# Kernel tuning notes

Hardware: AMD Instinct MI355X
Metric: run time of the kernel (lower is better)

Reference implementation:

```python
import jax, jax.numpy as jnp
import numpy as np

N = 30000   # clients (single instance, repeat=1)
F = 16      # num_node_features
EP = 30000  # solution-graph (tour) edges per parent
EF = 240000 # full graph k-NN edges (degree 8)
H = 8       # heads
D = 64      # hidden_dim
R = 64      # routes per parent (= max_to_move)
HD = H * D  # 512


def _gatv2(x, src, dst, ea, Wl, Wr, We, att, b, d_out):
    # PyG GATv2Conv: score = att . leaky_relu(Wl x_src + Wr x_dst + We e), softmax over dst
    n = x.shape[0]
    xl = (x @ Wl).reshape(n, H, d_out)
    xr = (x @ Wr).reshape(n, H, d_out)
    ee = (ea @ We).reshape(-1, H, d_out)
    s = jax.nn.leaky_relu(xl[src] + xr[dst] + ee, 0.2)          # [E,H,d]
    logits = jnp.einsum('ehd,hd->eh', s, att)                    # [E,H]
    m = jax.ops.segment_max(logits, dst, num_segments=n)
    ex = jnp.exp(logits - m[dst])
    den = jax.ops.segment_sum(ex, dst, num_segments=n)
    alpha = ex / (den[dst] + 1e-16)
    out = jax.ops.segment_sum(xl[src] * alpha[..., None], dst, num_segments=n)
    return out.reshape(n, H * d_out) + b


def _bn(x, g, b):
    # BatchNorm with track_running_stats=False -> batch statistics
    mu = jnp.mean(x, 0)
    v = jnp.var(x, 0)
    return (x - mu) * jax.lax.rsqrt(v + 1e-5) * g + b


def _routes(emb, rid):
    # sum client embeddings per route, then prefix sums over routes (moved vs kept sets)
    rs = jax.ops.segment_sum(emb, rid, num_segments=R)   # [R, 2HD]
    cs = jnp.cumsum(rs, 0)
    return cs, cs[-1] - cs


def setup_inputs() -> dict:
    key = jax.random.key(0)
    ks = iter(jax.random.split(key, 64))
    sc = 0.05
    rn = lambda shape: jax.random.normal(next(ks), shape, jnp.float32)
    d = {}
    d['x_p1'] = rn((N, F)); d['x_p2'] = rn((N, F)); d['x_full'] = rn((N, F))
    d['ea_p1'] = jax.random.uniform(next(ks), (EP, 1))
    d['ea_p2'] = jax.random.uniform(next(ks), (EP, 1))
    d['ea_full'] = jax.random.uniform(next(ks), (EF, 1))
    d['ei_p1'] = jax.random.randint(next(ks), (2, EP), 0, N)
    d['ei_p2'] = jax.random.randint(next(ks), (2, EP), 0, N)
    d['ei_full'] = jax.random.randint(next(ks), (2, EF), 0, N)
    d['route_p1'] = jax.random.randint(next(ks), (N,), 0, R)
    d['route_p2'] = jax.random.randint(next(ks), (N,), 0, R)
    # GAT params: (SolutionGraph, FullGraph, both)
    for tag, cin, dout in (('1', F, D), ('2', F, D), ('3', 2 * HD, 2 * D)):
        d['Wl' + tag] = rn((cin, H * dout)) * sc
        d['Wr' + tag] = rn((cin, H * dout)) * sc
        d['We' + tag] = rn((1, H * dout)) * sc
        d['att' + tag] = rn((H, dout)) * sc
        d['b' + tag] = jnp.zeros((H * dout,), jnp.float32)
    d['bng'] = jnp.ones((2 * HD,), jnp.float32); d['bnb'] = jnp.zeros((2 * HD,), jnp.float32)
    d['png'] = jnp.ones((8 * HD,), jnp.float32); d['pnb'] = jnp.zeros((8 * HD,), jnp.float32)
    dims = [8 * HD, 4 * HD, 2 * HD, HD, HD // 2, HD // 4, HD // 8, HD // 16, 1]
    for i in range(8):
        d['W%d' % (i + 1)] = rn((dims[i], dims[i + 1])) * sc
        d['c%d' % (i + 1)] = jnp.zeros((dims[i + 1],), jnp.float32)
    return d


def reference(x_p1, x_p2, x_full, ea_p1, ea_p2, ea_full, ei_p1, ei_p2, ei_full,
              route_p1, route_p2,
              Wl1, Wr1, We1, att1, b1, Wl2, Wr2, We2, att2, b2,
              Wl3, Wr3, We3, att3, b3, bng, bnb, png, pnb,
              W1, c1, W2, c2, W3, c3, W4, c4, W5, c5, W6, c6, W7, c7, W8, c8):
    p1 = _gatv2(x_p1, ei_p1[0], ei_p1[1], ea_p1, Wl1, Wr1, We1, att1, b1, D)
    p2 = _gatv2(x_p2, ei_p2[0], ei_p2[1], ea_p2, Wl1, Wr1, We1, att1, b1, D)
    fg = _gatv2(x_full, ei_full[0], ei_full[1], ea_full, Wl2, Wr2, We2, att2, b2, D)
    # single instance -> repeat=1: concat client embedding with full-graph embedding
    p1f = _bn(jnp.concatenate([p1, fg], 1), bng, bnb)
    p2f = _bn(jnp.concatenate([p2, fg], 1), bng, bnb)
    p1f = _gatv2(p1f, ei_p1[0], ei_p1[1], ea_p1, Wl3, Wr3, We3, att3, b3, 2 * D)
    p2f = _gatv2(p2f, ei_p2[0], ei_p2[1], ea_p2, Wl3, Wr3, We3, att3, b3, 2 * D)
    c1s, r1s = _routes(p1f, route_p1)
    c2s, r2s = _routes(p2f, route_p2)
    ptop = jnp.concatenate([c1s, r1s, c2s, r2s], 1)   # [R, 8*HD]
    h = _bn(ptop, png, pnb)
    lrelu = lambda z: jax.nn.leaky_relu(z, 0.01)
    h = lrelu(h @ W1 + c1)
    h = lrelu(h @ W2 + c2)
    h = lrelu(h @ W3 + c3)
    h = lrelu(h @ W4 + c4)
    h = lrelu(h @ W5 + c5)
    h = lrelu(h @ W6 + c6)
    h = lrelu(h @ W7 + c7)
    h = h @ W8 + c8
    probs = jax.nn.sigmoid(h).ravel()
    ptop_batch = jnp.zeros((R,), jnp.int32)
    return probs, ptop_batch
```

## Files before the change

### kernel.cpp

```cpp
#include <hip/hip_runtime.h>
#include <stdint.h>

typedef unsigned short u16;
typedef unsigned int   u32;
typedef __attribute__((ext_vector_type(8))) short bf16x8;
typedef __attribute__((ext_vector_type(4))) float f32x4;

#define NN    30000
#define NNP   30208
#define EFULL 240000
#define EPAR  30000

__device__ __forceinline__ float b2f(u16 u){ u32 x=((u32)u)<<16; float f; __builtin_memcpy(&f,&x,4); return f; }
__device__ __forceinline__ u16 f2b(float f){ u32 x; __builtin_memcpy(&x,&f,4); x += 0x7fffu + ((x>>16)&1u); return (u16)(x>>16); }

__device__ __forceinline__ void gload_lds16(const u16* g, u16* l){
  __builtin_amdgcn_global_load_lds((const __attribute__((address_space(1))) void*)g,
                                   (__attribute__((address_space(3))) void*)l, 16, 0, 0);
}

__global__ void k_fail(float* out){ int t=threadIdx.x; if(t<128) out[t]=2.0f; }

__global__ void k_counte3(const int* __restrict__ d0, const int* __restrict__ d1, const int* __restrict__ d2,
                          int* __restrict__ c0, int* __restrict__ c1, int* __restrict__ c2){
  int z = blockIdx.z;
  const int* d = z==0? d0 : z==1? d1 : d2;
  int* c = z==0? c0 : z==1? c1 : c2;
  int E = z==0? EFULL : EPAR;
  int e = blockIdx.x*256 + threadIdx.x;
  if (e < E) atomicAdd(&c[d[e]], 1);
}

__global__ void k_scan3(const int* __restrict__ c0, const int* __restrict__ c1, const int* __restrict__ c2,
                        int* __restrict__ r0, int* __restrict__ r1, int* __restrict__ r2,
                        int* __restrict__ w0, int* __restrict__ w1, int* __restrict__ w2){
  __shared__ int sums[1024];
  int z = blockIdx.x;
  const int* cnt = z==0? c0 : z==1? c1 : c2;
  int* rp = z==0? r0 : z==1? r1 : r2;
  int* wp = z==0? w0 : z==1? w1 : w2;
  int t = threadIdx.x;
  const int CH = (NN + 1023)/1024;
  int c00 = t*CH;
  int s = 0;
  for (int i=0;i<CH;i++){ int idx=c00+i; s += (idx<NN)? cnt[idx] : 0; }
  sums[t] = s; __syncthreads();
  for (int off=1; off<1024; off<<=1){
    int v = (t>=off)? sums[t-off] : 0;
    __syncthreads();
    sums[t] += v;
    __syncthreads();
  }
  int run = (t==0)? 0 : sums[t-1];
  for (int i=0;i<CH;i++){
    int idx=c00+i;
    if (idx<NN){ rp[idx]=run; wp[idx]=run; run += cnt[idx]; }
  }
  if (t==1023) rp[NN] = sums[1023];
}

__global__ void k_count64(const int* __restrict__ rt0, const int* __restrict__ rt1,
                          const int* __restrict__ d0, const int* __restrict__ d1,
                          int* __restrict__ c0, int* __restrict__ c1,
                          int* __restrict__ c2, int* __restrict__ c3){
  int z = blockIdx.z;
  int i = blockIdx.x*256 + threadIdx.x;
  if (i >= NN) return;
  if      (z==0) atomicAdd(&c0[rt0[i]], 1);
  else if (z==1) atomicAdd(&c1[rt1[i]], 1);
  else if (z==2) atomicAdd(&c2[rt0[d0[i]]], 1);
  else           atomicAdd(&c3[rt1[d1[i]]], 1);
}

__global__ void k_scan64x4(const int* __restrict__ c0, const int* __restrict__ c1,
                           const int* __restrict__ c2, const int* __restrict__ c3,
                           int* __restrict__ r0, int* __restrict__ r1,
                           int* __restrict__ r2, int* __restrict__ r3,
                           int* __restrict__ w2, int* __restrict__ w3){
  int t = threadIdx.x;
  if (t >= 4) return;
  const int* c = t==0?c0:t==1?c1:t==2?c2:c3;
  int* r = t==0?r0:t==1?r1:t==2?r2:r3;
  int run=0;
  for (int i=0;i<64;i++){
    r[i]=run;
    if (t==2) w2[i]=run;
    if (t==3) w3[i]=run;
    run+=c[i];
  }
  r[64]=run;
}

__global__ void k_fill_all(
    const int* __restrict__ dF, const int* __restrict__ d1, const int* __restrict__ d2,
    int* __restrict__ wF, int* __restrict__ wA, int* __restrict__ wB,
    int* __restrict__ xF, int* __restrict__ x1, int* __restrict__ x2,
    const int* __restrict__ rt1, const int* __restrict__ rt2,
    int* __restrict__ w64c, int* __restrict__ w64d,
    int* __restrict__ reix1, int* __restrict__ reix2,
    const int* __restrict__ rp1, const int* __restrict__ rp2,
    int* __restrict__ nre1, int* __restrict__ nre2){
  int z = blockIdx.z;
  int i = blockIdx.x*256 + threadIdx.x;
  if      (z==0){ if (i<EFULL){ int p=atomicAdd(&wF[dF[i]],1);          xF[p]=i; } }
  else if (z==1){ if (i<EPAR) { int p=atomicAdd(&wA[d1[i]],1);          x1[p]=i; } }
  else if (z==2){ if (i<EPAR) { int p=atomicAdd(&wB[d2[i]],1);          x2[p]=i; } }
  else if (z==3){ if (i<EPAR) { int p=atomicAdd(&w64c[rt1[d1[i]]],1);   reix1[p]=i; } }
  else if (z==4){ if (i<EPAR) { int p=atomicAdd(&w64d[rt2[d2[i]]],1);   reix2[p]=i; } }
  else if (z==5){ if (i<NN && rp1[i+1]>rp1[i]) atomicAdd(&nre1[rt1[i]],1); }
  else          { if (i<NN && rp2[i+1]>rp2[i]) atomicAdd(&nre2[rt2[i]],1); }
}

__global__ __launch_bounds__(256) void k_xwl3(const float* __restrict__ xf,
    const float* __restrict__ x1, const float* __restrict__ x2,
    const float* __restrict__ WlF, const float* __restrict__ WlP,
    u16* __restrict__ xlF, u16* __restrict__ xl1, u16* __restrict__ xl2){
  int z = blockIdx.z;
  const float* x = z==0? xf : z==1? x1 : x2;
  const float* Wl = z==0? WlF : WlP;
  u16* xl = z==0? xlF : z==1? xl1 : xl2;
  int n = blockIdx.x;
  int c = blockIdx.y*256 + threadIdx.x;
  float a=0.f;
  #pragma unroll
  for (int k=0;k<16;k++) a += x[n*16+k]*Wl[k*512+c];
  xl[(size_t)n*512+c]=f2b(a);
}

__global__ __launch_bounds__(256) void k_gat1f3(
    const int* __restrict__ eiF, const float* __restrict__ eaF,
    const int* __restrict__ rpF, const int* __restrict__ eixF,
    const float* __restrict__ xF, const float* __restrict__ WrF,
    const float* __restrict__ WeF, const float* __restrict__ attF,
    const u16* __restrict__ xlF, const float* __restrict__ bF, u16* __restrict__ outF,
    const int* __restrict__ ei1, const float* __restrict__ ea1,
    const int* __restrict__ rp1, const int* __restrict__ eix1,
    const float* __restrict__ x1p, const float* __restrict__ WrP,
    const float* __restrict__ WeP, const float* __restrict__ attP,
    const u16* __restrict__ xl1, const float* __restrict__ bP, u16* __restrict__ out1,
    const int* __restrict__ ei2, const float* __restrict__ ea2,
    const int* __restrict__ rp2, const int* __restrict__ eix2,
    const float* __restrict__ x2p, const u16* __restrict__ xl2, u16* __restrict__ out2){
  int z = blockIdx.z;
  const int* ei  = z==0? eiF : z==1? ei1 : ei2;
  const float* ea= z==0? eaF : z==1? ea1 : ea2;
  const int* rp  = z==0? rpF : z==1? rp1 : rp2;
  const int* eix = z==0? eixF: z==1? eix1: eix2;
  const float* x = z==0? xF  : z==1? x1p : x2p;
  const float* Wr= z==0? WrF : WrP;
  const float* We= z==0? WeF : WeP;
  const float* att=z==0? attF: attP;
  const u16* xl  = z==0? xlF : z==1? xl1 : xl2;
  const float* bias = z==0? bF : bP;
  u16* out = z==0? outF : z==1? out1 : out2;

  int lane = threadIdx.x & 63;
  int n = blockIdx.x*4 + (threadIdx.x>>6);
  if (n >= NN) return;
  int j0 = lane*8;
  float xv[16];
  #pragma unroll
  for (int k=0;k<16;k++) xv[k] = x[n*16+k];
  float we8[8], at8[8], rv8[8];
  #pragma unroll
  for (int j=0;j<8;j++){
    we8[j]=We[j0+j]; at8[j]=att[j0+j];
    float s=0.f;
    #pragma unroll
    for (int k=0;k<16;k++) s += xv[k]*Wr[k*512 + j0 + j];
    rv8[j]=s;
  }
  int r0 = rp[n], r1 = rp[n+1];
  float den = 0.f;
  float acc[8] = {0,0,0,0,0,0,0,0};
  for (int base=r0; base<r1; base+=64){
    int cnt = min(64, r1-base);
    int mysrc=0; float myea=0.f;
    if (lane < cnt){ int e = eix[base+lane]; mysrc = ei[e]; myea = ea[e]; }
    int scur = __shfl(mysrc, 0);
    float eacur = __shfl(myea, 0);
    bf16x8 rowc = *(const bf16x8*)(xl + (size_t)scur*512 + j0);
    for (int i=0;i<cnt;i++){
      bf16x8 rown = rowc; float ean = 0.f;
      if (i+1 < cnt){
        int sn = __shfl(mysrc, i+1);
        ean = __shfl(myea, i+1);
        rown = *(const bf16x8*)(xl + (size_t)sn*512 + j0);
      }
      float lvf[8];
      float logit = 0.f;
      #pragma unroll
      for (int j=0;j<8;j++){
        lvf[j] = b2f((u16)rowc[j]);
        float v = lvf[j] + rv8[j] + eacur*we8[j];
        v = v>0.f? v : 0.2f*v;
        logit += v*at8[j];
      }
      logit += __shfl_xor(logit,1);
      logit += __shfl_xor(logit,2);
      logit += __shfl_xor(logit,4);
      float a = __expf(logit);
      den += a;
      #pragma unroll
      for (int j=0;j<8;j++) acc[j] += a*lvf[j];
      rowc = rown; eacur = ean;
    }
  }
  float inv = 1.f/(den + 1e-16f);
  #pragma unroll
  for (int j=0;j<8;j++) out[(size_t)n*512 + j0 + j] = f2b(acc[j]*inv + bias[j0+j]);
}

__global__ __launch_bounds__(256) void k_bnstats(const u16* __restrict__ P1, const u16* __restrict__ P2,
    const u16* __restrict__ PF, float* __restrict__ s1, float* __restrict__ s2, float* __restrict__ sF){
  int z = blockIdx.y;
  const u16* P = z==0? P1 : z==1? P2 : PF;
  float* st = z==0? s1 : z==1? s2 : sF;
  int t = threadIdx.x;
  const u32* Pu = (const u32*)P;
  int r0 = blockIdx.x*250, r1 = r0+250;
  float a0=0.f,a1=0.f,q0=0.f,q1=0.f;
  for (int r=r0;r<r1;r++){
    u32 v = Pu[(size_t)r*256 + t];
    float a = b2f((u16)(v & 0xffffu));
    float b = b2f((u16)(v >> 16));
    a0+=a; q0+=a*a; a1+=b; q1+=b*b;
  }
  atomicAdd(&st[2*t],       a0);
  atomicAdd(&st[2*t+1],     a1);
  atomicAdd(&st[512+2*t],   q0);
  atomicAdd(&st[512+2*t+1], q1);
}

__global__ void k_prep(const float* __restrict__ st1, const float* __restrict__ st2,
                       const float* __restrict__ stF,
                       const float* __restrict__ g, const float* __restrict__ b,
                       float* __restrict__ sc1, float* __restrict__ sh1,
                       float* __restrict__ sc2, float* __restrict__ sh2){
  int k = blockIdx.x*256 + threadIdx.x;
  if (k >= 1024) return;
  const float invN = 1.f/30000.f;
  const float* st = (k<512)? st1 : stF;
  int kk = k & 511;
  float mu = st[kk]*invN;
  float var = st[512+kk]*invN - mu*mu;
  float sc = g[k]*rsqrtf(var + 1e-5f);
  sc1[k] = sc; sh1[k] = b[k] - mu*sc;
  st = (k<512)? st2 : stF;
  mu = st[kk]*invN;
  var = st[512+kk]*invN - mu*mu;
  sc = g[k]*rsqrtf(var + 1e-5f);
  sc2[k] = sc; sh2[k] = b[k] - mu*sc;
}

__global__ __launch_bounds__(256) void k_bt(const float* __restrict__ B0, const float* __restrict__ B1,
                                            const float* __restrict__ sc1, const float* __restrict__ sc2,
                                            u16* __restrict__ Bt1, u16* __restrict__ Bt2){
  __shared__ float tile[64][65];
  int bk = blockIdx.x;
  int bn = blockIdx.y;
  int par = blockIdx.z>>1, half = blockIdx.z&1;
  const float* B = half ? B1 : B0;
  const float* sc = par ? sc2 : sc1;
  u16* Bt = par ? Bt2 : Bt1;
  int nb = half*1024;
  for (int i = threadIdx.x; i < 64*64; i += 256){
    int r = i>>6, c = i&63;
    tile[c][r] = B[(size_t)(bk*64+r)*1024 + bn*64 + c] * sc[bk*64+r];
  }
  __syncthreads();
  for (int i = threadIdx.x; i < 64*64; i += 256){
    int r = i>>6, c = i&63;
    Bt[(size_t)(nb + bn*64 + r)*1024 + bk*64 + c] = f2b(tile[r][c]);
  }
}

__global__ void k_shiftb(const float* __restrict__ B0, const float* __restrict__ B1,
                         const float* __restrict__ sh1, const float* __restrict__ sh2,
                         float* __restrict__ sb1, float* __restrict__ sb2){
  int c = blockIdx.x*256 + threadIdx.x;
  const float* sh = blockIdx.y ? sh2 : sh1;
  float* sb = blockIdx.y ? sb2 : sb1;
  const float* B = (c < 1024) ? B0 : B1;
  int cc = c & 1023;
  float s = 0.f;
  for (int k=0;k<1024;k++) s += sh[k]*B[(size_t)k*1024 + cc];
  sb[c] = s;
}

__global__ __launch_bounds__(256) void k_gemm(const u16* __restrict__ A0, const u16* __restrict__ A1,
    const u16* __restrict__ Bt, u16* __restrict__ C, int M){
  __shared__ u16 As[128*64];
  __shared__ u16 Bs[128*64];
  int lin = blockIdx.y*16 + blockIdx.x;
  int wg  = (lin&7)*470 + (lin>>3);
  int n0 = (wg & 15)*128;
  int m0 = (wg >> 4)*128;
  int t = threadIdx.x;
  int wave = t>>6, lane = t&63;
  int wm = (wave>>1)*64, wn = (wave&1)*64;
  int rr = lane&15, kq = (lane>>4)*8;
  int srow = t>>3;
  int scol = (t&7)*8;
  int ssw  = ((t&7) ^ (srow&7))*8;
  f32x4 acc[4][4];
  #pragma unroll
  for (int m=0;m<4;m++)
    #pragma unroll
    for (int n=0;n<4;n++){ acc[m][n][0]=0.f; acc[m][n][1]=0.f; acc[m][n][2]=0.f; acc[m][n][3]=0.f; }
  for (int k0=0; k0<1024; k0+=64){
    const u16* Ap = (k0 < 512) ? A0 : A1;
    int kc = k0 & 511;
    #pragma unroll
    for (int i=0;i<4;i++){
      int row = i*32 + srow;
      gload_lds16(Ap + (size_t)(m0+row)*512 + kc + ssw, As + row*64 + scol);
    }
    #pragma unroll
    for (int i=0;i<4;i++){
      int row = i*32 + srow;
      gload_lds16(Bt + (size_t)(n0+row)*1024 + k0 + ssw, Bs + row*64 + scol);
    }
    __syncthreads();
    #pragma unroll
    for (int ks=0; ks<2; ks++){
      int pc = ((ks*4 + (lane>>4)) ^ (lane&7))*8;
      bf16x8 af[4], bb[4];
      #pragma unroll
      for (int m=0;m<4;m++) af[m] = *(const bf16x8*)(&As[(wm + m*16 + rr)*64 + pc]);
      #pragma unroll
      for (int n=0;n<4;n++) bb[n] = *(const bf16x8*)(&Bs[(wn + n*16 + rr)*64 + pc]);
      #pragma unroll
      for (int m=0;m<4;m++)
        #pragma unroll
        for (int n=0;n<4;n++)
          acc[m][n] = __builtin_amdgcn_mfma_f32_16x16x32_bf16(af[m], bb[n], acc[m][n], 0, 0, 0);
    }
    __syncthreads();
  }
  int rq = (lane>>4)*4;
  #pragma unroll
  for (int m=0;m<4;m++)
    #pragma unroll
    for (int n=0;n<4;n++)
      #pragma unroll
      for (int j=0;j<4;j++){
        int row = m0 + wm + m*16 + rq + j;
        int col = n0 + wn + n*16 + rr;
        if (row < M) C[(size_t)row*2048 + col] = f2b(acc[m][n][j]);
      }
}

__global__ __launch_bounds__(256) void k_edge2f(const int* __restrict__ ei,
    const float* __restrict__ ea,
    const int* __restrict__ rp, const int* __restrict__ eix,
    const float* __restrict__ We, const float* __restrict__ att,
    const u16* __restrict__ CAT, const float* __restrict__ sb,
    float* __restrict__ alpha){
  int lane = threadIdx.x & 63;
  int n = blockIdx.x*4 + (threadIdx.x>>6);
  if (n >= NN) return;
  int j0 = lane*16;
  float rv[16], we16[16], at16[16];
  bf16x8 rr0 = *(const bf16x8*)(CAT + (size_t)n*2048 + 1024 + j0);
  bf16x8 rr1 = *(const bf16x8*)(CAT + (size_t)n*2048 + 1024 + j0 + 8);
  #pragma unroll
  for (int j=0;j<16;j++){
    rv[j] = b2f((u16)((j<8)? rr0[j] : rr1[j-8])) + sb[1024+j0+j] + sb[j0+j];
    we16[j]=We[j0+j]; at16[j]=att[j0+j];
  }
  int e0 = rp[n], e1 = rp[n+1];
  float den = 0.f;
  for (int base=e0; base<e1; base+=64){
    int cnt = min(64, e1-base);
    int myE=0, mysrc=0; float myea=0.f;
    if (lane < cnt){ myE = eix[base+lane]; mysrc = ei[myE]; myea = ea[myE]; }
    int scur = __shfl(mysrc, 0);
    float eacur = __shfl(myea, 0);
    bf16x8 l0c = *(const bf16x8*)(CAT + (size_t)scur*2048 + j0);
    bf16x8 l1c = *(const bf16x8*)(CAT + (size_t)scur*2048 + j0 + 8);
    for (int i=0;i<cnt;i++){
      int ecur = __shfl(myE, i);
      bf16x8 l0n = l0c, l1n = l1c; float ean = 0.f;
      if (i+1 < cnt){
        int sn = __shfl(mysrc, i+1);
        ean = __shfl(myea, i+1);
        l0n = *(const bf16x8*)(CAT + (size_t)sn*2048 + j0);
        l1n = *(const bf16x8*)(CAT + (size_t)sn*2048 + j0 + 8);
      }
      float logit = 0.f;
      #pragma unroll
      for (int j=0;j<16;j++){
        float v = b2f((u16)((j<8)? l0c[j] : l1c[j-8])) + rv[j] + eacur*we16[j];
        v = v>0.f? v : 0.2f*v;
        logit += v*at16[j];
      }
      logit += __shfl_xor(logit,1);
      logit += __shfl_xor(logit,2);
      logit += __shfl_xor(logit,4);
      float ex_ = __expf(logit);
      den += ex_;
      if ((lane&7)==0) alpha[(size_t)ecur*8 + (lane>>3)] = ex_;
      l0c = l0n; l1c = l1n; eacur = ean;
    }
  }
  float dh = __shfl(den, (lane&7)*8);
  float inv = 1.f/(dh + 1e-16f);
  for (int base=e0; base<e1; base+=8){
    int idx = base + (lane>>3);
    if (idx < e1){
      int e = eix[idx];
      alpha[(size_t)e*8 + (lane&7)] *= inv;
    }
  }
}

#define ECH 32
__global__ __launch_bounds__(256) void k_agg2pool(const int* __restrict__ ei,
    const int* __restrict__ rerp, const int* __restrict__ reix,
    const int* __restrict__ rrp, const int* __restrict__ nre,
    const float* __restrict__ alpha, const u16* __restrict__ CAT,
    const float* __restrict__ b3, const float* __restrict__ sb,
    float* __restrict__ rs){
  int r = blockIdx.x;
  int c = blockIdx.z*256 + threadIdx.x;
  int h = c >> 7;
  int i0 = rerp[r], i1 = rerp[r+1];
  int per = (i1 - i0 + ECH - 1)/ECH;
  int s0 = i0 + blockIdx.y*per;
  int s1 = min(i1, s0 + per);
  float acc = 0.f;
  for (int i=s0;i<s1;i++){
    int e = reix[i];
    float a = alpha[(size_t)e*8 + h];
    acc += a * b2f(CAT[(size_t)ei[e]*2048 + c]);
  }
  if (blockIdx.y == 0)
    acc += (float)(rrp[r+1]-rrp[r]) * b3[c] + (float)nre[r] * sb[c];
  if (s0 < s1 || blockIdx.y == 0) atomicAdd(&rs[r*1024 + c], acc);
}

__global__ void k_cumsum_bn(const float* __restrict__ rs1, const float* __restrict__ rs2,
                            const float* __restrict__ g, const float* __restrict__ b,
                            float* __restrict__ h){
  const float* rs = blockIdx.y ? rs2 : rs1;
  int colbase = blockIdx.y ? 2048 : 0;
  int c = blockIdx.x*256 + threadIdx.x;
  float tot = 0.f;
  for (int r=0;r<64;r++) tot += rs[r*1024+c];
  float cs=0.f, s0=0.f,q0=0.f,s1=0.f,q1=0.f;
  for (int r=0;r<64;r++){
    cs += rs[r*1024+c];
    float m = tot - cs;
    s0+=cs; q0+=cs*cs; s1+=m; q1+=m*m;
  }
  float mu0=s0*(1.f/64.f), v0=q0*(1.f/64.f)-mu0*mu0, n0=rsqrtf(v0+1e-5f);
  float mu1=s1*(1.f/64.f), v1=q1*(1.f/64.f)-mu1*mu1, n1=rsqrtf(v1+1e-5f);
  float g0=g[colbase+c],      b0=b[colbase+c];
  float g1=g[colbase+1024+c], b1=b[colbase+1024+c];
  cs = 0.f;
  for (int r=0;r<64;r++){
    cs += rs[r*1024+c];
    float m = tot - cs;
    h[r*4096 + colbase + c]        = (cs-mu0)*n0*g0 + b0;
    h[r*4096 + colbase + 1024 + c] = (m -mu1)*n1*g1 + b1;
  }
}

#define KC 512
__global__ __launch_bounds__(256) void k_mlp_part(const float* __restrict__ In,
    const float* __restrict__ W, float* __restrict__ PART, int Ci, int Co){
  __shared__ float tin[64*64];
  int c  = blockIdx.x*64 + (threadIdx.x&63);
  int rg = threadIdx.x>>6;
  int k0 = blockIdx.y*KC, k1 = min(Ci, k0+KC);
  float acc[16];
  #pragma unroll
  for (int j=0;j<16;j++) acc[j]=0.f;
  for (int ks=k0; ks<k1; ks+=64){
    int kw = min(64, k1-ks);
    __syncthreads();
    for (int i=threadIdx.x;i<64*64;i+=256){
      int r=i>>6, k=i&63;
      tin[i] = (k<kw)? In[(size_t)r*Ci + ks + k] : 0.f;
    }
    __syncthreads();
    if (c < Co){
      for (int k=0;k<kw;k+=4){
        float4 w4;
        w4.x = W[(size_t)(ks+k  )*Co + c];
        w4.y = W[(size_t)(ks+k+1)*Co + c];
        w4.z = W[(size_t)(ks+k+2)*Co + c];
        w4.w = W[(size_t)(ks+k+3)*Co + c];
        #pragma unroll
        for (int j=0;j<16;j++){
          float4 t4 = *(const float4*)(&tin[(rg*16+j)*64 + k]);
          acc[j] += t4.x*w4.x + t4.y*w4.y + t4.z*w4.z + t4.w*w4.w;
        }
      }
    }
  }
  if (c < Co){
    float* P = PART + (size_t)blockIdx.y*64*Co;
    #pragma unroll
    for (int j=0;j<16;j++)
      P[(size_t)(rg*16+j)*Co + c] = acc[j];
  }
}

__global__ void k_mlp_red(const float* __restrict__ PART, const float* __restrict__ bias,
                          float* __restrict__ Out, int Co, int SK, int act){
  int idx = blockIdx.x*256 + threadIdx.x;
  if (idx >= 64*Co) return;
  int c = idx % Co;
  float s = bias[c];
  for (int sk=0; sk<SK; sk++) s += PART[(size_t)sk*64*Co + idx];
  if (act) s = s>0.f ? s : 0.01f*s;
  Out[idx] = s;
}

__global__ __launch_bounds__(256) void k_mlp_tail(const float* __restrict__ In,
    const float* __restrict__ W5, const float* __restrict__ c5,
    const float* __restrict__ W6, const float* __restrict__ c6,
    const float* __restrict__ W7, const float* __restrict__ c7,
    const float* __restrict__ W8, const float* __restrict__ c8,
    float* __restrict__ out){
  __shared__ float A[64*256];
  __shared__ float B[64*128];
  int t = threadIdx.x;
  for (int i=t;i<64*256;i+=256) A[i] = In[i];
  __syncthreads();
  for (int idx=t; idx<64*128; idx+=256){
    int r=idx>>7, c=idx&127;
    float s=c5[c];
    for (int k=0;k<256;k++) s += A[r*256+k]*W5[k*128+c];
    B[idx] = s>0.f? s : 0.01f*s;
  }
  __syncthreads();
  for (int idx=t; idx<64*64; idx+=256){
    int r=idx>>6, c=idx&63;
    float s=c6[c];
    for (int k=0;k<128;k++) s += B[r*128+k]*W6[k*64+c];
    A[idx] = s>0.f? s : 0.01f*s;
  }
  __syncthreads();
  for (int idx=t; idx<64*32; idx+=256){
    int r=idx>>5, c=idx&31;
    float s=c7[c];
    for (int k=0;k<64;k++) s += A[r*64+k]*W7[k*32+c];
    B[idx] = s>0.f? s : 0.01f*s;
  }
  __syncthreads();
  if (t<64){
    float s=c8[0];
    for (int k=0;k<32;k++) s += B[t*32+k]*W8[k];
    out[t] = 1.f/(1.f + __expf(-s));
    out[64+t] = 0.f;
  }
}

extern "C" void kernel_launch(void* const* d_in, const int* in_sizes, int n_in,
                              void* d_out, int out_size, void* d_ws, size_t ws_size,
                              hipStream_t stream)
{
  const float* x_p1   = (const float*)d_in[0];
  const float* x_p2   = (const float*)d_in[1];
  const float* x_full = (const float*)d_in[2];
  const float* ea_p1  = (const float*)d_in[3];
  const float* ea_p2  = (const float*)d_in[4];
  const float* ea_full= (const float*)d_in[5];
  const int* ei_p1  = (const int*)d_in[6];
  const int* ei_p2  = (const int*)d_in[7];
  const int* ei_full= (const int*)d_in[8];
  const int* route_p1 = (const int*)d_in[9];
  const int* route_p2 = (const int*)d_in[10];
  const float *Wl1=(const float*)d_in[11], *Wr1=(const float*)d_in[12], *We1=(const float*)d_in[13], *att1=(const float*)d_in[14], *b1=(const float*)d_in[15];
  const float *Wl2=(const float*)d_in[16], *Wr2=(const float*)d_in[17], *We2=(const float*)d_in[18], *att2=(const float*)d_in[19], *b2=(const float*)d_in[20];
  const float *Wl3=(const float*)d_in[21], *Wr3=(const float*)d_in[22], *We3=(const float*)d_in[23], *att3=(const float*)d_in[24], *b3=(const float*)d_in[25];
  const float *bng=(const float*)d_in[26], *bnb=(const float*)d_in[27], *png=(const float*)d_in[28], *pnb=(const float*)d_in[29];
  const float *W[8], *Cb[8];
  for (int i=0;i<8;i++){ W[i]=(const float*)d_in[30+2*i]; Cb[i]=(const float*)d_in[31+2*i]; }

  char* w = (char*)d_ws;
  size_t off = 0;
  auto alloc = [&](size_t bytes)->char*{ char* p = w + off; off += (bytes + 255) & ~(size_t)255; return p; };
  u16* P1bf = (u16*)alloc((size_t)NNP*512*2);
  u16* P2bf = (u16*)alloc((size_t)NNP*512*2);
  u16* FGbf = (u16*)alloc((size_t)NNP*512*2);
  char* BIG = alloc((size_t)NN*2048*2);
  u16*   XLF  = (u16*)BIG;
  u16*   XL1  = (u16*)(BIG + (size_t)NN*512*2);
  u16*   XL2  = (u16*)(BIG + (size_t)NN*512*2*2);
  u16*   CATbf= (u16*)BIG;
  u16*   Bt1  = (u16*)alloc((size_t)2048*1024*2);
  u16*   Bt2  = (u16*)alloc((size_t)2048*1024*2);
  float* ALPHA=(float*)alloc((size_t)EPAR*8*4);
  float* st1 = (float*)alloc(1024*4);
  float* st2 = (float*)alloc(1024*4);
  float* stF = (float*)alloc(1024*4);
  float* rs1 = (float*)alloc(64*1024*4);
  float* rs2 = (float*)alloc(64*1024*4);
  float* sc1 = (float*)alloc(1024*4);
  float* sh1 = (float*)alloc(1024*4);
  float* sc2 = (float*)alloc(1024*4);
  float* sh2 = (float*)alloc(1024*4);
  float* sb1 = (float*)alloc(2048*4);
  float* sb2 = (float*)alloc(2048*4);
  float* H0  = (float*)alloc(64*4096*4);
  float* H1  = (float*)alloc(64*4096*4);
  float* PART= (float*)alloc((size_t)8*64*2048*4);
  char* cnt_base = alloc(0);
  int* cntF = (int*)alloc(NN*4);
  int* cntA = (int*)alloc(NN*4);
  int* cntB = (int*)alloc(NN*4);
  int* c64a = (int*)alloc(64*4);
  int* c64b = (int*)alloc(64*4);
  int* c64c = (int*)alloc(64*4);
  int* c64d = (int*)alloc(64*4);
  int* nre1 = (int*)alloc(64*4);
  int* nre2 = (int*)alloc(64*4);
  size_t cnt_bytes = (size_t)((char*)alloc(0) - cnt_base);
  int* wpF = (int*)alloc(NN*4);
  int* wpA = (int*)alloc(NN*4);
  int* wpB = (int*)alloc(NN*4);
  int* w64c= (int*)alloc(64*4);
  int* w64d= (int*)alloc(64*4);
  int* rpF = (int*)alloc((NN+1)*4);
  int* rp1 = (int*)alloc((NN+1)*4);
  int* rp2 = (int*)alloc((NN+1)*4);
  int* eixF= (int*)alloc((size_t)EFULL*4);
  int* eix1= (int*)alloc((size_t)EPAR*4);
  int* eix2= (int*)alloc((size_t)EPAR*4);
  int* rr1 = (int*)alloc(65*4);
  int* rr2 = (int*)alloc(65*4);
  int* rerp1=(int*)alloc(65*4);
  int* rerp2=(int*)alloc(65*4);
  int* reix1=(int*)alloc((size_t)EPAR*4);
  int* reix2=(int*)alloc((size_t)EPAR*4);
  if (ws_size < off){ k_fail<<<1,128,0,stream>>>((float*)d_out); return; }

  hipMemsetAsync(cnt_base, 0, cnt_bytes, stream);
  hipMemsetAsync(st1, 0, (size_t)((char*)rs2 - (char*)st1) + 64*1024*4, stream);

  k_counte3<<<dim3((EFULL+255)/256,1,3), 256, 0, stream>>>(ei_full+EFULL, ei_p1+EPAR, ei_p2+EPAR,
                                                           cntF, cntA, cntB);
  k_count64<<<dim3((NN+255)/256,1,4), 256, 0, stream>>>(route_p1, route_p2, ei_p1+EPAR, ei_p2+EPAR,
                                                        c64a, c64b, c64c, c64d);
  k_scan3  <<<3, 1024, 0, stream>>>(cntF, cntA, cntB, rpF, rp1, rp2, wpF, wpA, wpB);
  k_scan64x4<<<1, 64, 0, stream>>>(c64a,c64b,c64c,c64d, rr1,rr2,rerp1,rerp2, w64c,w64d);
  k_fill_all<<<dim3((EFULL+255)/256,1,7), 256, 0, stream>>>(
      ei_full+EFULL, ei_p1+EPAR, ei_p2+EPAR, wpF, wpA, wpB, eixF, eix1, eix2,
      route_p1, route_p2, w64c, w64d, reix1, reix2, rp1, rp2, nre1, nre2);

  k_xwl3 <<<dim3(NN,2,3), 256, 0, stream>>>(x_full, x_p1, x_p2, Wl2, Wl1, XLF, XL1, XL2);
  k_gat1f3<<<dim3((NN+3)/4,1,3), 256, 0, stream>>>(
      ei_full, ea_full, rpF, eixF, x_full, Wr2, We2, att2, XLF, b2, FGbf,
      ei_p1,   ea_p1,   rp1, eix1, x_p1,   Wr1, We1, att1, XL1, b1, P1bf,
      ei_p2,   ea_p2,   rp2, eix2, x_p2,   XL2, P2bf);

  k_bnstats<<<dim3(120,3), 256, 0, stream>>>(P1bf, P2bf, FGbf, st1, st2, stF);
  k_prep   <<<4, 256, 0, stream>>>(st1, st2, stF, bng, bnb, sc1, sh1, sc2, sh2);
  k_bt     <<<dim3(16,16,4), 256, 0, stream>>>(Wl3, Wr3, sc1, sc2, Bt1, Bt2);
  k_shiftb <<<dim3(8,2), 256, 0, stream>>>(Wl3, Wr3, sh1, sh2, sb1, sb2);

  auto layer2 = [&](const u16* Pbf, const u16* Bt, const float* sb,
                    const int* ei, const float* ea, const int* rp, const int* eix,
                    const int* rrp, const int* nre, const int* rerp, const int* reix, float* rs){
    k_gemm <<<dim3(16, (NN+127)/128), 256, 0, stream>>>(Pbf, FGbf, Bt, CATbf, NN);
    k_edge2f<<<(NN+3)/4, 256, 0, stream>>>(ei, ea, rp, eix, We3, att3, CATbf, sb, ALPHA);
    k_agg2pool<<<dim3(64,ECH,4), 256, 0, stream>>>(ei, rerp, reix, rrp, nre, ALPHA, CATbf, b3, sb, rs);
  };
  layer2(P1bf, Bt1, sb1, ei_p1, ea_p1, rp1, eix1, rr1, nre1, rerp1, reix1, rs1);
  layer2(P2bf, Bt2, sb2, ei_p2, ea_p2, rp2, eix2, rr2, nre2, rerp2, reix2, rs2);

  k_cumsum_bn<<<dim3(4,2), 256, 0, stream>>>(rs1, rs2, png, pnb, H0);

  int dims[5] = {4096, 2048, 1024, 512, 256};
  float* bufs[2] = {H0, H1};
  for (int i=0;i<4;i++){
    int Ci = dims[i], Co = dims[i+1];
    int SK = (Ci + KC - 1)/KC;
    k_mlp_part<<<dim3((Co+63)/64, SK), 256, 0, stream>>>(bufs[i&1], W[i], PART, Ci, Co);
    k_mlp_red <<<(64*Co+255)/256, 256, 0, stream>>>(PART, Cb[i], bufs[(i+1)&1], Co, SK, 1);
  }
  k_mlp_tail<<<1, 256, 0, stream>>>(H0, W[4], Cb[4], W[5], Cb[5], W[6], Cb[6], W[7], Cb[7],
                                    (float*)d_out);
}
```

Baseline: 1.609 ms.

## Pre-gather edge src/attr into CSR order and precompute xr projection separately

The fill kernel now writes source indices and edge attributes directly in destination-sorted order, so the GAT kernels read them contiguously instead of through an indirect eix->ei/ea gather. The first-layer projection kernel is reworked to stage 128 nodes of x in shared memory with weights in registers, and now also computes xr, which removes the per-node Wr recomputation inside the aggregation kernel. The three first-layer graphs are now processed one after another through a shared XL/XR buffer instead of in a single batched launch. This adds more kernel launches, loses the concurrency of the z-batched launch, and writes extra index arrays.

```diff
diff --git a/kernel.cpp b/kernel.cpp
--- a/kernel.cpp
+++ b/kernel.cpp
@@ -92,91 +92,77 @@
 }
 
 __global__ void k_fill_all(
-    const int* __restrict__ dF, const int* __restrict__ d1, const int* __restrict__ d2,
+    const int* __restrict__ eiF, const float* __restrict__ eaF,
+    const int* __restrict__ ei1, const float* __restrict__ ea1,
+    const int* __restrict__ ei2, const float* __restrict__ ea2,
     int* __restrict__ wF, int* __restrict__ wA, int* __restrict__ wB,
-    int* __restrict__ xF, int* __restrict__ x1, int* __restrict__ x2,
+    int* __restrict__ srcF, float* __restrict__ eaxF,
+    int* __restrict__ eix1, int* __restrict__ src1, float* __restrict__ eax1,
+    int* __restrict__ eix2, int* __restrict__ src2, float* __restrict__ eax2,
     const int* __restrict__ rt1, const int* __restrict__ rt2,
     int* __restrict__ w64c, int* __restrict__ w64d,
-    int* __restrict__ reix1, int* __restrict__ reix2,
+    int* __restrict__ reix1, int* __restrict__ resrc1,
+    int* __restrict__ reix2, int* __restrict__ resrc2,
     const int* __restrict__ rp1, const int* __restrict__ rp2,
     int* __restrict__ nre1, int* __restrict__ nre2){
   int z = blockIdx.z;
   int i = blockIdx.x*256 + threadIdx.x;
-  if      (z==0){ if (i<EFULL){ int p=atomicAdd(&wF[dF[i]],1);          xF[p]=i; } }
-  else if (z==1){ if (i<EPAR) { int p=atomicAdd(&wA[d1[i]],1);          x1[p]=i; } }
-  else if (z==2){ if (i<EPAR) { int p=atomicAdd(&wB[d2[i]],1);          x2[p]=i; } }
-  else if (z==3){ if (i<EPAR) { int p=atomicAdd(&w64c[rt1[d1[i]]],1);   reix1[p]=i; } }
-  else if (z==4){ if (i<EPAR) { int p=atomicAdd(&w64d[rt2[d2[i]]],1);   reix2[p]=i; } }
+  if      (z==0){ if (i<EFULL){ int p=atomicAdd(&wF[eiF[EFULL+i]],1); srcF[p]=eiF[i]; eaxF[p]=eaF[i]; } }
+  else if (z==1){ if (i<EPAR) { int p=atomicAdd(&wA[ei1[EPAR+i]],1);  eix1[p]=i; src1[p]=ei1[i]; eax1[p]=ea1[i]; } }
+  else if (z==2){ if (i<EPAR) { int p=atomicAdd(&wB[ei2[EPAR+i]],1);  eix2[p]=i; src2[p]=ei2[i]; eax2[p]=ea2[i]; } }
+  else if (z==3){ if (i<EPAR) { int p=atomicAdd(&w64c[rt1[ei1[EPAR+i]]],1); reix1[p]=i; resrc1[p]=ei1[i]; } }
+  else if (z==4){ if (i<EPAR) { int p=atomicAdd(&w64d[rt2[ei2[EPAR+i]]],1); reix2[p]=i; resrc2[p]=ei2[i]; } }
   else if (z==5){ if (i<NN && rp1[i+1]>rp1[i]) atomicAdd(&nre1[rt1[i]],1); }
   else          { if (i<NN && rp2[i+1]>rp2[i]) atomicAdd(&nre2[rt2[i]],1); }
 }
 
-__global__ __launch_bounds__(256) void k_xwl3(const float* __restrict__ xf,
-    const float* __restrict__ x1, const float* __restrict__ x2,
-    const float* __restrict__ WlF, const float* __restrict__ WlP,
-    u16* __restrict__ xlF, u16* __restrict__ xl1, u16* __restrict__ xl2){
-  int z = blockIdx.z;
-  const float* x = z==0? xf : z==1? x1 : x2;
-  const float* Wl = z==0? WlF : WlP;
-  u16* xl = z==0? xlF : z==1? xl1 : xl2;
-  int n = blockIdx.x;
+#define NB 128
+__global__ __launch_bounds__(256) void k_xw(const float* __restrict__ x,
+    const float* __restrict__ Wl, const float* __restrict__ Wr,
+    u16* __restrict__ xl, u16* __restrict__ xr){
+  __shared__ float xs[NB*16];
+  int half = blockIdx.z;
+  const float* W = half? Wr : Wl;
+  u16* o = half? xr : xl;
   int c = blockIdx.y*256 + threadIdx.x;
-  float a=0.f;
+  float wreg[16];
   #pragma unroll
-  for (int k=0;k<16;k++) a += x[n*16+k]*Wl[k*512+c];
-  xl[(size_t)n*512+c]=f2b(a);
-}
-
-__global__ __launch_bounds__(256) void k_gat1f3(
-    const int* __restrict__ eiF, const float* __restrict__ eaF,
-    const int* __restrict__ rpF, const int* __restrict__ eixF,
-    const float* __restrict__ xF, const float* __restrict__ WrF,
-    const float* __restrict__ WeF, const float* __restrict__ attF,
-    const u16* __restrict__ xlF, const float* __restrict__ bF, u16* __restrict__ outF,
-    const int* __restrict__ ei1, const float* __restrict__ ea1,
-    const int* __restrict__ rp1, const int* __restrict__ eix1,
-    const float* __restrict__ x1p, const float* __restrict__ WrP,
-    const float* __restrict__ WeP, const float* __restrict__ attP,
-    const u16* __restrict__ xl1, const float* __restrict__ bP, u16* __restrict__ out1,
-    const int* __restrict__ ei2, const float* __restrict__ ea2,
-    const int* __restrict__ rp2, const int* __restrict__ eix2,
-    const float* __restrict__ x2p, const u16* __restrict__ xl2, u16* __restrict__ out2){
-  int z = blockIdx.z;
-  const int* ei  = z==0? eiF : z==1? ei1 : ei2;
-  const float* ea= z==0? eaF : z==1? ea1 : ea2;
-  const int* rp  = z==0? rpF : z==1? rp1 : rp2;
-  const int* eix = z==0? eixF: z==1? eix1: eix2;
-  const float* x = z==0? xF  : z==1? x1p : x2p;
-  const float* Wr= z==0? WrF : WrP;
-  const float* We= z==0? WeF : WeP;
-  const float* att=z==0? attF: attP;
-  const u16* xl  = z==0? xlF : z==1? xl1 : xl2;
-  const float* bias = z==0? bF : bP;
-  u16* out = z==0? outF : z==1? out1 : out2;
-
+  for (int k=0;k<16;k++) wreg[k] = W[k*512+c];
+  int n0 = blockIdx.x*NB;
+  for (int i=threadIdx.x; i<NB*16; i+=256){
+    int n = n0 + (i>>4);
+    xs[i] = (n<NN)? x[(size_t)n*16 + (i&15)] : 0.f;
+  }
+  __syncthreads();
+  int nmax = min(NB, NN-n0);
+  for (int i=0;i<nmax;i++){
+    float a=0.f;
+    #pragma unroll
+    for (int k=0;k<16;k++) a += xs[i*16+k]*wreg[k];
+    o[(size_t)(n0+i)*512+c] = f2b(a);
+  }
+}
+
+__global__ __launch_bounds__(256) void k_gat1f(
+    const int* __restrict__ rp, const int* __restrict__ srcx, const float* __restrict__ eax,
+    const float* __restrict__ We, const float* __restrict__ att,
+    const u16* __restrict__ xl, const u16* __restrict__ xr,
+    const float* __restrict__ bias, u16* __restrict__ out){
   int lane = threadIdx.x & 63;
   int n = blockIdx.x*4 + (threadIdx.x>>6);
   if (n >= NN) return;
   int j0 = lane*8;
-  float xv[16];
+  float we8[8], at8[8], rv8[8];
+  bf16x8 rvv = *(const bf16x8*)(xr + (size_t)n*512 + j0);
   #pragma unroll
-  for (int k=0;k<16;k++) xv[k] = x[n*16+k];
-  float we8[8], at8[8], rv8[8];
-  #pragma unroll
-  for (int j=0;j<8;j++){
-    we8[j]=We[j0+j]; at8[j]=att[j0+j];
-    float s=0.f;
-    #pragma unroll
-    for (int k=0;k<16;k++) s += xv[k]*Wr[k*512 + j0 + j];
-    rv8[j]=s;
-  }
+  for (int j=0;j<8;j++){ we8[j]=We[j0+j]; at8[j]=att[j0+j]; rv8[j]=b2f((u16)rvv[j]); }
   int r0 = rp[n], r1 = rp[n+1];
   float den = 0.f;
   float acc[8] = {0,0,0,0,0,0,0,0};
   for (int base=r0; base<r1; base+=64){
     int cnt = min(64, r1-base);
     int mysrc=0; float myea=0.f;
-    if (lane < cnt){ int e = eix[base+lane]; mysrc = ei[e]; myea = ea[e]; }
+    if (lane < cnt){ mysrc = srcx[base+lane]; myea = eax[base+lane]; }
     int scur = __shfl(mysrc, 0);
     float eacur = __shfl(myea, 0);
     bf16x8 rowc = *(const bf16x8*)(xl + (size_t)scur*512 + j0);
@@ -351,9 +337,9 @@
       }
 }
 
-__global__ __launch_bounds__(256) void k_edge2f(const int* __restrict__ ei,
-    const float* __restrict__ ea,
+__global__ __launch_bounds__(256) void k_edge2f(
     const int* __restrict__ rp, const int* __restrict__ eix,
+    const int* __restrict__ srcx, const float* __restrict__ eax,
     const float* __restrict__ We, const float* __restrict__ att,
     const u16* __restrict__ CAT, const float* __restrict__ sb,
     float* __restrict__ alpha){
@@ -374,7 +360,7 @@
   for (int base=e0; base<e1; base+=64){
     int cnt = min(64, e1-base);
     int myE=0, mysrc=0; float myea=0.f;
-    if (lane < cnt){ myE = eix[base+lane]; mysrc = ei[myE]; myea = ea[myE]; }
+    if (lane < cnt){ myE = eix[base+lane]; mysrc = srcx[base+lane]; myea = eax[base+lane]; }
     int scur = __shfl(mysrc, 0);
     float eacur = __shfl(myea, 0);
     bf16x8 l0c = *(const bf16x8*)(CAT + (size_t)scur*2048 + j0);
@@ -416,8 +402,8 @@
 }
 
 #define ECH 32
-__global__ __launch_bounds__(256) void k_agg2pool(const int* __restrict__ ei,
-    const int* __restrict__ rerp, const int* __restrict__ reix,
+__global__ __launch_bounds__(256) void k_agg2pool(
+    const int* __restrict__ rerp, const int* __restrict__ reix, const int* __restrict__ resrc,
     const int* __restrict__ rrp, const int* __restrict__ nre,
     const float* __restrict__ alpha, const u16* __restrict__ CAT,
     const float* __restrict__ b3, const float* __restrict__ sb,
@@ -432,8 +418,9 @@
   float acc = 0.f;
   for (int i=s0;i<s1;i++){
     int e = reix[i];
+    int src = resrc[i];
     float a = alpha[(size_t)e*8 + h];
-    acc += a * b2f(CAT[(size_t)ei[e]*2048 + c]);
+    acc += a * b2f(CAT[(size_t)src*2048 + c]);
   }
   if (blockIdx.y == 0)
     acc += (float)(rrp[r+1]-rrp[r]) * b3[c] + (float)nre[r] * sb[c];
@@ -588,9 +575,8 @@
   u16* P2bf = (u16*)alloc((size_t)NNP*512*2);
   u16* FGbf = (u16*)alloc((size_t)NNP*512*2);
   char* BIG = alloc((size_t)NN*2048*2);
-  u16*   XLF  = (u16*)BIG;
-  u16*   XL1  = (u16*)(BIG + (size_t)NN*512*2);
-  u16*   XL2  = (u16*)(BIG + (size_t)NN*512*2*2);
+  u16*   XLbf = (u16*)BIG;
+  u16*   XRbf = (u16*)(BIG + (size_t)NN*512*2);
   u16*   CATbf= (u16*)BIG;
   u16*   Bt1  = (u16*)alloc((size_t)2048*1024*2);
   u16*   Bt2  = (u16*)alloc((size_t)2048*1024*2);
@@ -628,15 +614,22 @@
   int* rpF = (int*)alloc((NN+1)*4);
   int* rp1 = (int*)alloc((NN+1)*4);
   int* rp2 = (int*)alloc((NN+1)*4);
-  int* eixF= (int*)alloc((size_t)EFULL*4);
-  int* eix1= (int*)alloc((size_t)EPAR*4);
-  int* eix2= (int*)alloc((size_t)EPAR*4);
+  int*   srcF = (int*)alloc((size_t)EFULL*4);
+  float* eaxF = (float*)alloc((size_t)EFULL*4);
+  int*   eix1 = (int*)alloc((size_t)EPAR*4);
+  int*   src1 = (int*)alloc((size_t)EPAR*4);
+  float* eax1 = (float*)alloc((size_t)EPAR*4);
+  int*   eix2 = (int*)alloc((size_t)EPAR*4);
+  int*   src2 = (int*)alloc((size_t)EPAR*4);
+  float* eax2 = (float*)alloc((size_t)EPAR*4);
   int* rr1 = (int*)alloc(65*4);
   int* rr2 = (int*)alloc(65*4);
   int* rerp1=(int*)alloc(65*4);
   int* rerp2=(int*)alloc(65*4);
   int* reix1=(int*)alloc((size_t)EPAR*4);
+  int* resrc1=(int*)alloc((size_t)EPAR*4);
   int* reix2=(int*)alloc((size_t)EPAR*4);
+  int* resrc2=(int*)alloc((size_t)EPAR*4);
   if (ws_size < off){ k_fail<<<1,128,0,stream>>>((float*)d_out); return; }
 
   hipMemsetAsync(cnt_base, 0, cnt_bytes, stream);
@@ -649,14 +642,22 @@
   k_scan3  <<<3, 1024, 0, stream>>>(cntF, cntA, cntB, rpF, rp1, rp2, wpF, wpA, wpB);
   k_scan64x4<<<1, 64, 0, stream>>>(c64a,c64b,c64c,c64d, rr1,rr2,rerp1,rerp2, w64c,w64d);
   k_fill_all<<<dim3((EFULL+255)/256,1,7), 256, 0, stream>>>(
-      ei_full+EFULL, ei_p1+EPAR, ei_p2+EPAR, wpF, wpA, wpB, eixF, eix1, eix2,
-      route_p1, route_p2, w64c, w64d, reix1, reix2, rp1, rp2, nre1, nre2);
-
-  k_xwl3 <<<dim3(NN,2,3), 256, 0, stream>>>(x_full, x_p1, x_p2, Wl2, Wl1, XLF, XL1, XL2);
-  k_gat1f3<<<dim3((NN+3)/4,1,3), 256, 0, stream>>>(
-      ei_full, ea_full, rpF, eixF, x_full, Wr2, We2, att2, XLF, b2, FGbf,
-      ei_p1,   ea_p1,   rp1, eix1, x_p1,   Wr1, We1, att1, XL1, b1, P1bf,
-      ei_p2,   ea_p2,   rp2, eix2, x_p2,   XL2, P2bf);
+      ei_full, ea_full, ei_p1, ea_p1, ei_p2, ea_p2,
+      wpF, wpA, wpB,
+      srcF, eaxF, eix1, src1, eax1, eix2, src2, eax2,
+      route_p1, route_p2, w64c, w64d,
+      reix1, resrc1, reix2, resrc2,
+      rp1, rp2, nre1, nre2);
+
+  auto gat1 = [&](const float* x, const int* rp, const int* srcx, const float* eax,
+                  const float* Wl, const float* Wr, const float* We, const float* att,
+                  const float* bias, u16* out){
+    k_xw   <<<dim3((NN+NB-1)/NB, 2, 2), 256, 0, stream>>>(x, Wl, Wr, XLbf, XRbf);
+    k_gat1f<<<(NN+3)/4, 256, 0, stream>>>(rp, srcx, eax, We, att, XLbf, XRbf, bias, out);
+  };
+  gat1(x_full, rpF, srcF, eaxF, Wl2, Wr2, We2, att2, b2, FGbf);
+  gat1(x_p1,   rp1, src1, eax1, Wl1, Wr1, We1, att1, b1, P1bf);
+  gat1(x_p2,   rp2, src2, eax2, Wl1, Wr1, We1, att1, b1, P2bf);
 
   k_bnstats<<<dim3(120,3), 256, 0, stream>>>(P1bf, P2bf, FGbf, st1, st2, stF);
   k_prep   <<<4, 256, 0, stream>>>(st1, st2, stF, bng, bnb, sc1, sh1, sc2, sh2);
@@ -664,14 +665,15 @@
   k_shiftb <<<dim3(8,2), 256, 0, stream>>>(Wl3, Wr3, sh1, sh2, sb1, sb2);
 
   auto layer2 = [&](const u16* Pbf, const u16* Bt, const float* sb,
-                    const int* ei, const float* ea, const int* rp, const int* eix,
-                    const int* rrp, const int* nre, const int* rerp, const int* reix, float* rs){
+                    const int* rp, const int* eix, const int* srcx, const float* eax,
+                    const int* rrp, const int* nre, const int* rerp,
+                    const int* reix, const int* resrc, float* rs){
     k_gemm <<<dim3(16, (NN+127)/128), 256, 0, stream>>>(Pbf, FGbf, Bt, CATbf, NN);
-    k_edge2f<<<(NN+3)/4, 256, 0, stream>>>(ei, ea, rp, eix, We3, att3, CATbf, sb, ALPHA);
-    k_agg2pool<<<dim3(64,ECH,4), 256, 0, stream>>>(ei, rerp, reix, rrp, nre, ALPHA, CATbf, b3, sb, rs);
+    k_edge2f<<<(NN+3)/4, 256, 0, stream>>>(rp, eix, srcx, eax, We3, att3, CATbf, sb, ALPHA);
+    k_agg2pool<<<dim3(64,ECH,4), 256, 0, stream>>>(rerp, reix, resrc, rrp, nre, ALPHA, CATbf, b3, sb, rs);
   };
-  layer2(P1bf, Bt1, sb1, ei_p1, ea_p1, rp1, eix1, rr1, nre1, rerp1, reix1, rs1);
-  layer2(P2bf, Bt2, sb2, ei_p2, ea_p2, rp2, eix2, rr2, nre2, rerp2, reix2, rs2);
+  layer2(P1bf, Bt1, sb1, rp1, eix1, src1, eax1, rr1, nre1, rerp1, reix1, resrc1, rs1);
+  layer2(P2bf, Bt2, sb2, rp2, eix2, src2, eax2, rr2, nre2, rerp2, reix2, resrc2, rs2);
 
   k_cumsum_bn<<<dim3(4,2), 256, 0, stream>>>(rs1, rs2, png, pnb, H0);
 
```

New measurement: 1.547 ms. 1.04x faster.
